# Kernel tuning notes

Hardware: AMD Instinct MI355X
Metric: run time of the kernel (lower is better)

The kernel has to match this reference:

```python
import jax, jax.numpy as jnp
from jax import lax
import numpy as np


def setup_inputs() -> dict:
    key = jax.random.key(0)
    k1, k2, k3, k4 = jax.random.split(key, 4)
    X = jax.random.normal(k1, (2_000_000, 20), dtype=jnp.float32)
    W = jax.random.normal(k2, (20, 20), dtype=jnp.float32) * 0.1  # Linear weight
    b = jax.random.normal(k3, (20,), dtype=jnp.float32) * 0.1     # Linear bias
    rand_weight = jax.random.uniform(k4, (20, 20), dtype=jnp.float32)  # fixed, non-trainable
    return {"X": X, "W": W, "b": b, "rand_weight": rand_weight}


def reference(X, W, b, rand_weight):
    # X = self.liner(X)  -> torch Linear: X @ W.T + b
    h = X @ W.T + b
    # X = relu(X @ rand_weight + 1)
    h = jax.nn.relu(h @ rand_weight + 1.0)
    # (second self.liner(X) in the source is computed but unused -> omitted)
    # while X.abs().sum() > 1: X /= 2  -- count halvings, then apply once.
    s0 = jnp.sum(jnp.abs(h))
    def cond(c):
        _, s = c
        return s > 1.0
    def body(c):
        n, s = c
        return n + 1, s * 0.5
    n, _ = lax.while_loop(cond, body, (jnp.int32(0), s0))
    h = h * jnp.exp2(-n.astype(h.dtype))  # exact power-of-two scaling == repeated /2
    return jnp.sum(h)
```

## Files before the change

kernel.cpp:

```cpp
#include <hip/hip_runtime.h>


#define D 20
#define BLOCK 256
#define RPT 2
#define RPB (BLOCK * RPT)
#define WS_PARTIALS_BYTES 32768


__global__ void setup_kernel(const float* __restrict__ W,
                             const float* __restrict__ b,
                             const float* __restrict__ RW,
                             float* __restrict__ Mt,
                             float* __restrict__ dvec,
                             unsigned* __restrict__ counter) {
    const int tid = threadIdx.x;
    if (tid == 0) *counter = 0u;
    for (int idx = tid; idx < D * D; idx += blockDim.x) {
        const int j = idx / D, k = idx % D;
        float s = 0.0f;
        for (int i = 0; i < D; ++i)
            s = fmaf(W[i * D + k], RW[i * D + j], s);
        Mt[idx] = s;
    }
    if (tid < D) {
        float s = 1.0f;
        for (int i = 0; i < D; ++i)
            s = fmaf(b[i], RW[i * D + tid], s);
        dvec[tid] = s;
    }
}

__global__ void __launch_bounds__(BLOCK)
fused_mlp_sum(const float* __restrict__ X,
              const float* __restrict__ Mt,
              const float* __restrict__ dvec,
              double* __restrict__ partials,
              unsigned* __restrict__ counter,
              float* __restrict__ out,
              int nrows) {
    __shared__ float wave_sums[BLOCK / 64];
    __shared__ double dsum[BLOCK / 64];
    __shared__ int is_last;

    const int tid  = threadIdx.x;
    const int lane = tid & 63;
    const int wave = tid >> 6;
    const long long t = (long long)blockIdx.x * BLOCK + tid;
    const long long row0 = t * RPT;
    const bool valid = row0 < (long long)nrows;
    const long long rbase = valid ? row0 : (long long)nrows - RPT;
    const float* xp = X + rbase * D;

    float x0[D], x1[D];
#pragma unroll
    for (int q = 0; q < 5; ++q) {
        float4 v = ((const float4*)xp)[q];
        x0[4 * q + 0] = v.x; x0[4 * q + 1] = v.y;
        x0[4 * q + 2] = v.z; x0[4 * q + 3] = v.w;
        float4 u = ((const float4*)(xp + D))[q];
        x1[4 * q + 0] = u.x; x1[4 * q + 1] = u.y;
        x1[4 * q + 2] = u.z; x1[4 * q + 3] = u.w;
    }

    float lsum = 0.0f;
#pragma unroll
    for (int j = 0; j < D; ++j) {
        float t0 = dvec[j];
        float t1 = t0;
#pragma unroll
        for (int k = 0; k < D; ++k) {
            const float m = Mt[j * D + k];
            t0 = fmaf(x0[k], m, t0);
            t1 = fmaf(x1[k], m, t1);
        }
        lsum += fmaxf(t0, 0.0f) + fmaxf(t1, 0.0f);
    }
    lsum = valid ? lsum : 0.0f;

#pragma unroll
    for (int off = 32; off > 0; off >>= 1)
        lsum += __shfl_down(lsum, off, 64);
    if (lane == 0) wave_sums[wave] = lsum;
    __syncthreads();

    if (tid == 0) {
        const float bs = wave_sums[0] + wave_sums[1] + wave_sums[2] + wave_sums[3];
        __hip_atomic_store(&partials[blockIdx.x], (double)bs, __ATOMIC_RELEASE,
                           __HIP_MEMORY_SCOPE_AGENT);
        const unsigned tk = __hip_atomic_fetch_add(counter, 1u, __ATOMIC_ACQ_REL,
                                                   __HIP_MEMORY_SCOPE_AGENT);
        is_last = (tk == gridDim.x - 1);
    }
    __syncthreads();

    if (is_last) {
        double sd = 0.0;
        for (int i = tid; i < (int)gridDim.x; i += BLOCK)
            sd += __hip_atomic_load(&partials[i], __ATOMIC_RELAXED,
                                    __HIP_MEMORY_SCOPE_AGENT);
#pragma unroll
        for (int off = 32; off > 0; off >>= 1)
            sd += __shfl_down(sd, off, 64);
        if (lane == 0) dsum[wave] = sd;
        __syncthreads();
        if (tid == 0) {
            const double s0 = dsum[0] + dsum[1] + dsum[2] + dsum[3];
            float f = (float)s0;
            while (f > 1.0f) f *= 0.5f;
            out[0] = f;
        }
    }
}

extern "C" void kernel_launch(void* const* d_in, const int* in_sizes, int n_in,
                              void* d_out, int out_size, void* d_ws, size_t ws_size,
                              hipStream_t stream) {
    const float* X  = (const float*)d_in[0];
    const float* W  = (const float*)d_in[1];
    const float* b  = (const float*)d_in[2];
    const float* RW = (const float*)d_in[3];
    float* out = (float*)d_out;

    double* partials = (double*)d_ws;
    float*  Mt = (float*)((char*)d_ws + WS_PARTIALS_BYTES);
    float*  dv = Mt + D * D;
    unsigned* counter = (unsigned*)((char*)d_ws + WS_PARTIALS_BYTES + 1600 + 80);

    const int nrows = in_sizes[0] / (D * 4);

    setup_kernel<<<1, 256, 0, stream>>>(W, b, RW, Mt, dv, counter);

    const long long nthreads = ((long long)nrows + RPT - 1) / RPT;
    const int blocks = (int)((nthreads + BLOCK - 1) / BLOCK);
    fused_mlp_sum<<<blocks, BLOCK, 0, stream>>>(X, Mt, dv, partials, counter,
                                                out, nrows);
}
```

Before: 229.0 us.

## Stage rows through LDS with coalesced float4 loads, one row per thread

Each wave now loads its 64 rows of X as contiguous float4s spread across lanes, so global reads are coalesced, then transposes them through shared memory so each thread reads its own row. Rows per thread drop from two to one, which doubles the grid, and the workspace for per-block partials grows to match. The final reduction over partials is unrolled into four accumulators. This adds an LDS round trip and more blocks, and the per-thread arithmetic gets less reuse of the weight loads across rows.

```diff
diff --git a/kernel.cpp b/kernel.cpp
--- a/kernel.cpp
+++ b/kernel.cpp
@@ -3,9 +3,10 @@
 
 #define D 20
 #define BLOCK 256
-#define RPT 2
-#define RPB (BLOCK * RPT)
-#define WS_PARTIALS_BYTES 32768
+#define WAVE_ROWS 64
+#define WAVE_F4 (WAVE_ROWS * D / 4)
+#define BLOCK_F4 (BLOCK * D / 4)
+#define WS_PARTIALS_BYTES 65536
 
 
 __global__ void setup_kernel(const float* __restrict__ W,
@@ -39,6 +40,7 @@
               unsigned* __restrict__ counter,
               float* __restrict__ out,
               int nrows) {
+    __shared__ float4 lds4[BLOCK_F4];
     __shared__ float wave_sums[BLOCK / 64];
     __shared__ double dsum[BLOCK / 64];
     __shared__ int is_last;
@@ -46,35 +48,43 @@
     const int tid  = threadIdx.x;
     const int lane = tid & 63;
     const int wave = tid >> 6;
-    const long long t = (long long)blockIdx.x * BLOCK + tid;
-    const long long row0 = t * RPT;
-    const bool valid = row0 < (long long)nrows;
-    const long long rbase = valid ? row0 : (long long)nrows - RPT;
-    const float* xp = X + rbase * D;
+    const int bid  = blockIdx.x;
 
-    float x0[D], x1[D];
+    const long long row = (long long)bid * BLOCK + tid;
+    const bool valid = row < (long long)nrows;
+
+    const long long max_f4 = (long long)nrows * (D / 4) - 1;
+    const long long wbase_f4 = (long long)bid * BLOCK_F4 + wave * WAVE_F4;
+    const float4* __restrict__ xg4 = (const float4*)X;
+    float4* const wl = lds4 + wave * WAVE_F4;
+
+    float4 st[5];
 #pragma unroll
     for (int q = 0; q < 5; ++q) {
-        float4 v = ((const float4*)xp)[q];
-        x0[4 * q + 0] = v.x; x0[4 * q + 1] = v.y;
-        x0[4 * q + 2] = v.z; x0[4 * q + 3] = v.w;
-        float4 u = ((const float4*)(xp + D))[q];
-        x1[4 * q + 0] = u.x; x1[4 * q + 1] = u.y;
-        x1[4 * q + 2] = u.z; x1[4 * q + 3] = u.w;
+        long long s = wbase_f4 + 64 * q + lane;
+        s = (s <= max_f4) ? s : max_f4;
+        st[q] = xg4[s];
+    }
+#pragma unroll
+    for (int q = 0; q < 5; ++q)
+        wl[64 * q + lane] = st[q];
+
+    float x[D];
+#pragma unroll
+    for (int q = 0; q < 5; ++q) {
+        const float4 v = wl[5 * lane + q];
+        x[4 * q + 0] = v.x; x[4 * q + 1] = v.y;
+        x[4 * q + 2] = v.z; x[4 * q + 3] = v.w;
     }
 
     float lsum = 0.0f;
 #pragma unroll
     for (int j = 0; j < D; ++j) {
-        float t0 = dvec[j];
-        float t1 = t0;
+        float t = dvec[j];
 #pragma unroll
-        for (int k = 0; k < D; ++k) {
-            const float m = Mt[j * D + k];
-            t0 = fmaf(x0[k], m, t0);
-            t1 = fmaf(x1[k], m, t1);
-        }
-        lsum += fmaxf(t0, 0.0f) + fmaxf(t1, 0.0f);
+        for (int k = 0; k < D; ++k)
+            t = fmaf(x[k], Mt[j * D + k], t);
+        lsum += fmaxf(t, 0.0f);
     }
     lsum = valid ? lsum : 0.0f;
 
@@ -86,7 +96,7 @@
 
     if (tid == 0) {
         const float bs = wave_sums[0] + wave_sums[1] + wave_sums[2] + wave_sums[3];
-        __hip_atomic_store(&partials[blockIdx.x], (double)bs, __ATOMIC_RELEASE,
+        __hip_atomic_store(&partials[bid], (double)bs, __ATOMIC_RELEASE,
                            __HIP_MEMORY_SCOPE_AGENT);
         const unsigned tk = __hip_atomic_fetch_add(counter, 1u, __ATOMIC_ACQ_REL,
                                                    __HIP_MEMORY_SCOPE_AGENT);
@@ -95,10 +105,23 @@
     __syncthreads();
 
     if (is_last) {
-        double sd = 0.0;
-        for (int i = tid; i < (int)gridDim.x; i += BLOCK)
-            sd += __hip_atomic_load(&partials[i], __ATOMIC_RELAXED,
+        const int G = (int)gridDim.x;
+        double a0 = 0.0, a1 = 0.0, a2 = 0.0, a3 = 0.0;
+        int i = tid;
+        for (; i + 3 * BLOCK < G; i += 4 * BLOCK) {
+            a0 += __hip_atomic_load(&partials[i], __ATOMIC_RELAXED,
                                     __HIP_MEMORY_SCOPE_AGENT);
+            a1 += __hip_atomic_load(&partials[i + BLOCK], __ATOMIC_RELAXED,
+                                    __HIP_MEMORY_SCOPE_AGENT);
+            a2 += __hip_atomic_load(&partials[i + 2 * BLOCK], __ATOMIC_RELAXED,
+                                    __HIP_MEMORY_SCOPE_AGENT);
+            a3 += __hip_atomic_load(&partials[i + 3 * BLOCK], __ATOMIC_RELAXED,
+                                    __HIP_MEMORY_SCOPE_AGENT);
+        }
+        for (; i < G; i += BLOCK)
+            a0 += __hip_atomic_load(&partials[i], __ATOMIC_RELAXED,
+                                    __HIP_MEMORY_SCOPE_AGENT);
+        double sd = (a0 + a1) + (a2 + a3);
 #pragma unroll
         for (int off = 32; off > 0; off >>= 1)
             sd += __shfl_down(sd, off, 64);
@@ -131,8 +154,7 @@
 
     setup_kernel<<<1, 256, 0, stream>>>(W, b, RW, Mt, dv, counter);
 
-    const long long nthreads = ((long long)nrows + RPT - 1) / RPT;
-    const int blocks = (int)((nthreads + BLOCK - 1) / BLOCK);
+    const int blocks = (nrows + BLOCK - 1) / BLOCK;
     fused_mlp_sum<<<blocks, BLOCK, 0, stream>>>(X, Mt, dv, partials, counter,
                                                 out, nrows);
 }
```

New measurement: 258.7 us. 1.13x slower.
